# Performance work log

Measured on AMD Instinct MI355X. Metric: run time of the kernel, lower is better.

The kernel has to match this reference:

```python
import jax, jax.numpy as jnp
import numpy as np

BATCH = 16384
N_IN = 128
CTX = 128
H = 1024
NB = 8                      # num_bins
OUT_MULT = 3 * NB - 1       # widths + heights + derivatives for RQS
TAIL = 3.0                  # tail_bound
SCALE = float(np.sqrt((H * H) // 2))  # sqrt(prod(hidden_dims)//len(hidden_dims))
MIN_W = 1e-3; MIN_H = 1e-3; MIN_D = 1e-3
DPAD = float(np.log(np.exp(1.0 - MIN_D) - 1.0))  # softplus(DPAD)+MIN_D == 1 at boundaries


def _masks():
    # Standard sequential MADE masks. Input degrees 1..n_in, hidden degrees cycle.
    deg_in = np.arange(1, N_IN + 1)
    deg_h = (np.arange(H) % (N_IN - 1)) + 1
    m0 = deg_h[:, None] >= deg_in[None, :]          # [H, N_IN]
    m1 = deg_h[:, None] >= deg_h[None, :]           # [H, H]
    deg_out = np.repeat(deg_in, OUT_MULT)           # matches view(b, n_in, out_mult)
    m2 = deg_out[:, None] > deg_h[None, :]          # [N_IN*OUT_MULT, H]
    return jnp.asarray(m0), jnp.asarray(m1), jnp.asarray(m2)


def setup_inputs() -> dict:
    key = jax.random.key(0)
    k = jax.random.split(key, 6)
    def rn(kk, shape, fan_in):
        return (jax.random.normal(kk, shape, dtype=jnp.float32) * np.sqrt(1.0 / fan_in)).astype(jnp.float32)
    m0, m1, m2 = _masks()
    return {
        "x": jax.random.normal(k[0], (BATCH, N_IN), dtype=jnp.float32),
        "context": jax.random.normal(k[1], (BATCH, CTX), dtype=jnp.float32),
        "ctx_w": rn(k[2], (H, CTX), CTX),
        "w0": rn(k[3], (H, N_IN), N_IN), "b0": jnp.zeros((H,), jnp.float32),
        "w1": rn(k[4], (H, H), H),       "b1": jnp.zeros((H,), jnp.float32),
        "w2": rn(k[5], (N_IN * OUT_MULT, H), H), "b2": jnp.zeros((N_IN * OUT_MULT,), jnp.float32),
        "mask0": m0, "mask1": m1, "mask2": m2,
    }


def _rqs(x, uw, uh, ud):
    # x: [B, D]; uw, uh: [B, D, NB]; ud: [B, D, NB-1]
    inside = jnp.abs(x) <= TAIL
    xc = jnp.clip(x, -TAIL, TAIL)

    w = MIN_W + (1.0 - MIN_W * NB) * jax.nn.softmax(uw, axis=-1)
    cw = jnp.cumsum(w, axis=-1)
    cw = jnp.concatenate([jnp.zeros_like(cw[..., :1]), cw], axis=-1)
    cw = 2.0 * TAIL * cw - TAIL
    cw = cw.at[..., 0].set(-TAIL).at[..., -1].set(TAIL)
    widths = cw[..., 1:] - cw[..., :-1]

    h = MIN_H + (1.0 - MIN_H * NB) * jax.nn.softmax(uh, axis=-1)
    ch = jnp.cumsum(h, axis=-1)
    ch = jnp.concatenate([jnp.zeros_like(ch[..., :1]), ch], axis=-1)
    ch = 2.0 * TAIL * ch - TAIL
    ch = ch.at[..., 0].set(-TAIL).at[..., -1].set(TAIL)
    heights = ch[..., 1:] - ch[..., :-1]

    pad = jnp.full(ud.shape[:-1] + (1,), DPAD, ud.dtype)
    d = MIN_D + jax.nn.softplus(jnp.concatenate([pad, ud, pad], axis=-1))  # [B, D, NB+1]

    # bucketize: bin index per element (NB is small; comparison-sum beats searchsorted here)
    idx = jnp.clip(jnp.sum((xc[..., None] >= cw).astype(jnp.int32), axis=-1) - 1, 0, NB - 1)
    g = lambda a, i: jnp.take_along_axis(a, i[..., None], axis=-1)[..., 0]

    in_cw = g(cw, idx); in_w = g(widths, idx)
    in_ch = g(ch, idx); in_h = g(heights, idx)
    delta = in_h / in_w
    d0 = g(d, idx); d1 = g(d, idx + 1)

    theta = (xc - in_cw) / in_w
    t1m = theta * (1.0 - theta)
    denom = delta + (d0 + d1 - 2.0 * delta) * t1m
    num = in_h * (delta * theta * theta + d0 * t1m)
    y = in_ch + num / denom
    logdet = (2.0 * jnp.log(delta)
              + jnp.log(d1 * theta * theta + 2.0 * delta * t1m + d0 * (1.0 - theta) ** 2)
              - 2.0 * jnp.log(denom))

    y = jnp.where(inside, y, x)          # identity linear tails
    logdet = jnp.where(inside, logdet, 0.0)
    return y, logdet


def reference(x, context, ctx_w, w0, b0, w1, b1, w2, b2, mask0, mask1, mask2):
    m0 = mask0.astype(w0.dtype); m1 = mask1.astype(w1.dtype); m2 = mask2.astype(w2.dtype)
    hdn = jax.nn.relu(context @ ctx_w.T + x @ (w0 * m0).T + b0)
    hdn = jax.nn.relu(hdn @ (w1 * m1).T + b1)
    out = (hdn @ (w2 * m2).T + b2).reshape(-1, N_IN, OUT_MULT)
    uw = out[..., :NB] / SCALE
    uh = out[..., NB:2 * NB] / SCALE
    ud = out[..., 2 * NB:]
    y, ld = _rqs(x, uw, uh, ud)
    return y, jnp.sum(ld, axis=-1)
```

## Files before the change

kernel.cpp:

```cpp
#include <hip/hip_runtime.h>
#include <cstdint>
#include <cstddef>

#define BATCH   16384
#define N_IN    128
#define CTX     128
#define HDIM    1024
#define NB      8
#define OUT_MULT 23
#define OUT_PAD 24
#define NOUTP   (N_IN * OUT_PAD)
#define KCAT    (CTX + N_IN)

typedef __bf16 bf16x8 __attribute__((ext_vector_type(8)));
typedef float  f32x4  __attribute__((ext_vector_type(4)));

__device__ __forceinline__ uint16_t f2bf(float f) {
    union { float f; uint32_t u; } v; v.f = f;
    uint32_t u = v.u;
    u += 0x7FFFu + ((u >> 16) & 1u);
    return (uint16_t)(u >> 16);
}

__device__ __forceinline__ int kpref_dev(int d) {
    return (d <= 8) ? 9 * d : 72 + 8 * (d - 8);
}
__device__ __forceinline__ int dpos_dev(int p) {
    return (p < 72) ? (p / 9) : (8 + ((p - 72) >> 3));
}
__device__ __forceinline__ int h_of(int p) {
    if (p < 72) { int d = p / 9, j = p - 9 * d; return d + 127 * j; }
    int q = p - 72; int d = 8 + (q >> 3); int j = q & 7; return d + 127 * j;
}

__device__ __forceinline__ void async_ld16(const void* g, const void* l) {
    __builtin_amdgcn_global_load_lds(
        (__attribute__((address_space(1))) void*)(uintptr_t)g,
        (__attribute__((address_space(3))) void*)(uint32_t)(uintptr_t)l,
        16, 0, 0);
}


__global__ void pack_all(
    const float* __restrict__ x,    const float* __restrict__ ctx,
    const float* __restrict__ ctx_w,const float* __restrict__ w0,
    const float* __restrict__ b0,   const float* __restrict__ w1,
    const float* __restrict__ b1,   const float* __restrict__ w2,
    const float* __restrict__ b2,
    uint16_t* __restrict__ xcat, uint16_t* __restrict__ wcat,
    uint16_t* __restrict__ w1m,  uint16_t* __restrict__ w2p,
    float* __restrict__ b0p, float* __restrict__ b1p, float* __restrict__ b2p,
    float* __restrict__ ldz)
{
    __shared__ float srow[HDIM];
    const int blk = blockIdx.x;
    const int tid = threadIdx.x;

    if (blk < 4096) {
        int idx4 = (blk * 256 + tid) * 4;
        int b = idx4 >> 8, c = idx4 & 255;
        f32x4 v = (c < CTX) ? *(const f32x4*)(ctx + (b << 7) + c)
                            : *(const f32x4*)(x   + (b << 7) + (c - CTX));
        ushort4 o;
        o.x = f2bf(v[0]); o.y = f2bf(v[1]); o.z = f2bf(v[2]); o.w = f2bf(v[3]);
        *(ushort4*)(xcat + idx4) = o;
    } else if (blk < 5120) {
        int idx = (blk - 4096) * 256 + tid;
        int p = idx >> 8, c = idx & 255;
        int h = h_of(p);
        float v;
        if (c < CTX) v = ctx_w[(h << 7) + c];
        else {
            int col = c - CTX;
            v = (dpos_dev(p) >= col) ? w0[(h << 7) + col] : 0.0f;
        }
        wcat[idx] = f2bf(v);
    } else if (blk < 6144) {
        const int po = blk - 5120;
        const int drow = dpos_dev(po);
        const float* src = w1 + (size_t)h_of(po) * HDIM;
        *((f32x4*)srow + tid) = *((const f32x4*)src + tid);
        __syncthreads();
        ushort4 o;
#pragma unroll
        for (int e = 0; e < 4; ++e) {
            int pi = 4 * tid + e;
            float v = (drow >= dpos_dev(pi)) ? srow[h_of(pi)] : 0.0f;
            ((uint16_t*)&o)[e] = f2bf(v);
        }
        *((ushort4*)(w1m + (size_t)po * HDIM) + tid) = o;
    } else if (blk < 9216) {
        const int oo = blk - 6144;
        const int g = oo / OUT_PAD, t = oo - g * OUT_PAD;
        const bool live = (t < OUT_MULT);
        if (live) {
            const float* src = w2 + (size_t)(g * OUT_MULT + t) * HDIM;
            *((f32x4*)srow + tid) = *((const f32x4*)src + tid);
        }
        __syncthreads();
        ushort4 o;
#pragma unroll
        for (int e = 0; e < 4; ++e) {
            int pi = 4 * tid + e;
            float v = (live && g > dpos_dev(pi)) ? srow[h_of(pi)] : 0.0f;
            ((uint16_t*)&o)[e] = f2bf(v);
        }
        *((ushort4*)(w2p + (size_t)oo * HDIM) + tid) = o;
    } else if (blk < 9232) {
        int idx = (blk - 9216) * 256 + tid;
        if (idx < HDIM) {
            int h = h_of(idx);
            b0p[idx] = b0[h];
            b1p[idx] = b1[h];
        } else {
            int oo = idx - HDIM;
            int g = oo / OUT_PAD, t = oo - g * OUT_PAD;
            b2p[oo] = (t < OUT_MULT) ? b2[g * OUT_MULT + t] : 0.0f;
        }
    } else {
        int idx = (blk - 9232) * 256 + tid;
        ldz[idx] = 0.0f;
    }
}


template<int MODE>
__device__ __forceinline__ void gemm_bt_body(
    const uint16_t* __restrict__ A,
    const uint16_t* __restrict__ B,
    const float*    __restrict__ bias,
    uint16_t*       __restrict__ C,
    int N, int K, int NT)
{
    __shared__ __align__(16) uint16_t sA[2][128 * 64];
    __shared__ __align__(16) uint16_t sB[2][128 * 64];

    const int GM    = 64;
    const int per   = GM * NT;
    const int id    = blockIdx.x;
    const int grp   = id / per;
    const int rem   = id - grp * per;
    const int mt    = grp * GM + (rem & (GM - 1));
    const int nt    = (NT - 1) - (rem >> 6);
    const int bm    = mt << 7;
    const int bn    = nt << 7;

    int K_eff;
    if (MODE == 0)      { int dmax = dpos_dev(bn + 127); K_eff = 128 + dmax + 1; }
    else                { int dmax = dpos_dev(bn + 127); K_eff = kpref_dev(dmax + 1); }
    K_eff = min(K, (K_eff + 63) & ~63);

    const int tid   = threadIdx.x;
    const int wid   = tid >> 6;
    const int lane  = tid & 63;
    const int wm    = (wid & 1) << 6;
    const int wn    = (wid >> 1) << 6;
    const int lrow  = lane & 15;
    const int lquad = lane >> 4;

    const f32x4 vzero = {0.0f, 0.0f, 0.0f, 0.0f};
    f32x4 acc[4][4];
#pragma unroll
    for (int i = 0; i < 4; ++i)
#pragma unroll
        for (int j = 0; j < 4; ++j) acc[i][j] = vzero;

    int goff[4];
#pragma unroll
    for (int t = 0; t < 4; ++t) {
        int c = t * 256 + tid;
        int row = c >> 3, j = c & 7;
        int oct = j ^ (row & 7);
        goff[t] = row * K * 2 + oct * 16;
    }
    const char* gA = (const char*)(A + (size_t)bm * K);
    const char* gB = (const char*)(B + (size_t)bn * K);

    const int octx = lrow & 7;

    auto stage = [&](int b, int k0) {
        const int kb = k0 * 2;
#pragma unroll
        for (int t = 0; t < 4; ++t) {
            const int ldsoff = (t * 256 + (wid << 6)) * 16;
            async_ld16(gA + goff[t] + kb, (const char*)sA[b] + ldsoff);
            async_ld16(gB + goff[t] + kb, (const char*)sB[b] + ldsoff);
        }
    };

    stage(0, 0);
    __syncthreads();

    int cur = 0;
    for (int k0 = 0; k0 < K_eff; k0 += 64) {
        if (k0 + 64 < K_eff) stage(cur ^ 1, k0 + 64);

        const uint16_t* rA = sA[cur] + (wm + lrow) * 64;
        const uint16_t* rB = sB[cur] + (wn + lrow) * 64;
#pragma unroll
        for (int ks = 0; ks < 2; ++ks) {
            const int oct = ((ks << 2) | lquad) ^ octx;
            bf16x8 af[4], bfr[4];
#pragma unroll
            for (int i = 0; i < 4; ++i) af[i]  = *(const bf16x8*)(rA + i * 1024 + oct * 8);
#pragma unroll
            for (int j = 0; j < 4; ++j) bfr[j] = *(const bf16x8*)(rB + j * 1024 + oct * 8);
#pragma unroll
            for (int i = 0; i < 4; ++i)
#pragma unroll
                for (int j = 0; j < 4; ++j)
                    acc[i][j] = __builtin_amdgcn_mfma_f32_16x16x32_bf16(
                                    af[i], bfr[j], acc[i][j], 0, 0, 0);
        }

        __syncthreads();
        cur ^= 1;
    }

#pragma unroll
    for (int j = 0; j < 4; ++j) {
        const int col = bn + wn + j * 16 + lrow;
        const float bv = bias[col];
#pragma unroll
        for (int i = 0; i < 4; ++i) {
            const int row0 = bm + wm + i * 16 + (lquad << 2);
#pragma unroll
            for (int r = 0; r < 4; ++r) {
                float v = fmaxf(acc[i][j][r] + bv, 0.0f);
                C[(size_t)(row0 + r) * N + col] = f2bf(v);
            }
        }
    }
}

__global__ __launch_bounds__(256, 2) void gemm1_k(
    const uint16_t* __restrict__ A, const uint16_t* __restrict__ B,
    const float* __restrict__ bias, uint16_t* __restrict__ C,
    int N, int K, int NT)
{ gemm_bt_body<0>(A, B, bias, C, N, K, NT); }

__global__ __launch_bounds__(256, 2) void gemm2_k(
    const uint16_t* __restrict__ A, const uint16_t* __restrict__ B,
    const float* __restrict__ bias, uint16_t* __restrict__ C,
    int N, int K, int NT)
{ gemm_bt_body<1>(A, B, bias, C, N, K, NT); }


__device__ __forceinline__ float frcp(float v) { return __builtin_amdgcn_rcpf(v); }
__device__ __forceinline__ float softplusf(float v) {
    return fmaxf(v, 0.0f) + __logf(1.0f + __expf(-fabsf(v)));
}

__device__ __forceinline__ void spline_eval(const float* __restrict__ pp,
                                            float xv, float& yout, float& ldout)
{
    float p[OUT_PAD];
#pragma unroll
    for (int k = 0; k < OUT_PAD / 4; ++k)
        *(f32x4*)(p + 4 * k) = *(const f32x4*)(pp + 4 * k);

    const float TAILF = 3.0f;
    const float MIN_W = 0.001f, MIN_H = 0.001f, MIN_D = 0.001f;
    const float INV_SCALE = 1.0f / 724.0773439350246f;

    const float xc = fminf(fmaxf(xv, -TAILF), TAILF);

    float uw[NB], uh[NB];
#pragma unroll
    for (int k = 0; k < NB; ++k) { uw[k] = p[k] * INV_SCALE; uh[k] = p[NB + k] * INV_SCALE; }
    float mw = uw[0], mh = uh[0];
#pragma unroll
    for (int k = 1; k < NB; ++k) { mw = fmaxf(mw, uw[k]); mh = fmaxf(mh, uh[k]); }
    float ew[NB], eh[NB], sw = 0.0f, sh = 0.0f;
#pragma unroll
    for (int k = 0; k < NB; ++k) {
        ew[k] = __expf(uw[k] - mw); sw += ew[k];
        eh[k] = __expf(uh[k] - mh); sh += eh[k];
    }
    const float FACW = (1.0f - MIN_W * NB) * frcp(sw);
    const float FACH = (1.0f - MIN_H * NB) * frcp(sh);

    float cw[NB + 1], ch[NB + 1];
    cw[0] = -TAILF; ch[0] = -TAILF;
    float aw = 0.0f, ah = 0.0f;
#pragma unroll
    for (int k = 0; k < NB; ++k) {
        aw += MIN_W + FACW * ew[k];
        ah += MIN_H + FACH * eh[k];
        cw[k + 1] = (k == NB - 1) ? TAILF : 2.0f * TAILF * aw - TAILF;
        ch[k + 1] = (k == NB - 1) ? TAILF : 2.0f * TAILF * ah - TAILF;
    }

    float dd[NB + 1];
    dd[0]  = 1.0f;
    dd[NB] = 1.0f;
#pragma unroll
    for (int k = 1; k < NB; ++k) dd[k] = MIN_D + softplusf(p[2 * NB + (k - 1)]);

    float in_cw = cw[0], cw_n = cw[1], in_ch = ch[0], ch_n = ch[1];
    float d0 = dd[0], d1 = dd[1];
#pragma unroll
    for (int k = 1; k < NB; ++k) {
        const bool ge = (xc >= cw[k]);
        in_cw = ge ? cw[k]     : in_cw;
        cw_n  = ge ? cw[k + 1] : cw_n;
        in_ch = ge ? ch[k]     : in_ch;
        ch_n  = ge ? ch[k + 1] : ch_n;
        d0    = ge ? dd[k]     : d0;
        d1    = ge ? dd[k + 1] : d1;
    }
    const float in_w  = cw_n - in_cw;
    const float in_h  = ch_n - in_ch;
    const float inv_w = frcp(in_w);
    const float delta = in_h * inv_w;
    const float theta = (xc - in_cw) * inv_w;
    const float omt   = 1.0f - theta;
    const float t1m   = theta * omt;
    const float denom = delta + (d0 + d1 - 2.0f * delta) * t1m;
    const float num   = in_h * (delta * theta * theta + d0 * t1m);
    float yv = in_ch + num * frcp(denom);
    float ld = 2.0f * __logf(delta)
             + __logf(d1 * theta * theta + 2.0f * delta * t1m + d0 * omt * omt)
             - 2.0f * __logf(denom);
    const bool inside = fabsf(xv) <= TAILF;
    yout  = inside ? yv : xv;
    ldout = inside ? ld : 0.0f;
}


__global__ __launch_bounds__(256, 2) void gemm3_spline(
    const uint16_t* __restrict__ A,
    const uint16_t* __restrict__ B,
    const float*    __restrict__ bias,
    const float*    __restrict__ x,
    float* __restrict__ y,
    float* __restrict__ ldsum)
{
    __shared__ __align__(16) char smem[57344];
    float* ep = (float*)smem;

    const int NT  = 32;
    const int per = 64 * NT;
    const int id  = blockIdx.x;
    const int grp = id / per;
    const int rem = id - grp * per;
    const int mt  = grp * 64 + (rem & 63);
    const int nt  = 31 - (rem >> 6);
    const int bm  = mt << 7;
    const int bn  = nt * 96;

    const int K = HDIM;
    int K_eff = kpref_dev(4 * nt + 3);
    K_eff = min(K, (K_eff + 63) & ~63);

    const int tid   = threadIdx.x;
    const int wid   = tid >> 6;
    const int lane  = tid & 63;
    const int wm    = (wid & 1) << 6;
    const int wn    = (wid >> 1) * 48;
    const int lrow  = lane & 15;
    const int lquad = lane >> 4;

    const f32x4 vzero = {0.0f, 0.0f, 0.0f, 0.0f};
    f32x4 acc[4][3];
#pragma unroll
    for (int i = 0; i < 4; ++i)
#pragma unroll
        for (int j = 0; j < 3; ++j) acc[i][j] = vzero;

    int goffA[4], goffB[3];
#pragma unroll
    for (int t = 0; t < 4; ++t) {
        int c = t * 256 + tid;
        int row = c >> 3, j = c & 7;
        goffA[t] = row * K * 2 + (j ^ (row & 7)) * 16;
    }
#pragma unroll
    for (int t = 0; t < 3; ++t) {
        int c = t * 256 + tid;
        int row = c >> 3, j = c & 7;
        goffB[t] = row * K * 2 + (j ^ (row & 7)) * 16;
    }
    const char* gA = (const char*)(A + (size_t)bm * K);
    const char* gB = (const char*)(B + (size_t)bn * K);

    const int octx = lrow & 7;

    auto stage = [&](int b, int k0) {
        const int kb = k0 * 2;
        char* dA = smem + b * 16384;
        char* dB = smem + 32768 + b * 12288;
#pragma unroll
        for (int t = 0; t < 4; ++t) {
            const int ldsoff = (t * 256 + (wid << 6)) * 16;
            async_ld16(gA + goffA[t] + kb, dA + ldsoff);
            if (t < 3)
                async_ld16(gB + goffB[t] + kb, dB + ldsoff);
        }
    };

    stage(0, 0);
    __syncthreads();

    int cur = 0;
    for (int k0 = 0; k0 < K_eff; k0 += 64) {
        if (k0 + 64 < K_eff) stage(cur ^ 1, k0 + 64);

        const uint16_t* rA = (const uint16_t*)(smem + cur * 16384)
                             + (wm + lrow) * 64;
        const uint16_t* rB = (const uint16_t*)(smem + 32768 + cur * 12288)
                             + (wn + lrow) * 64;
#pragma unroll
        for (int ks = 0; ks < 2; ++ks) {
            const int oct = ((ks << 2) | lquad) ^ octx;
            bf16x8 af[4], bfr[3];
#pragma unroll
            for (int i = 0; i < 4; ++i) af[i]  = *(const bf16x8*)(rA + i * 1024 + oct * 8);
#pragma unroll
            for (int j = 0; j < 3; ++j) bfr[j] = *(const bf16x8*)(rB + j * 1024 + oct * 8);
#pragma unroll
            for (int i = 0; i < 4; ++i)
#pragma unroll
                for (int j = 0; j < 3; ++j)
                    acc[i][j] = __builtin_amdgcn_mfma_f32_16x16x32_bf16(
                                    af[i], bfr[j], acc[i][j], 0, 0, 0);
        }

        __syncthreads();
        cur ^= 1;
    }

#pragma unroll
    for (int ph = 0; ph < 2; ++ph) {
        if ((wid & 1) == ph) {
#pragma unroll
            for (int j = 0; j < 3; ++j) {
                const int col = wn + j * 16 + lrow;
                const float bv = bias[bn + col];
#pragma unroll
                for (int i = 0; i < 4; ++i) {
                    const int r0 = i * 16 + (lquad << 2);
#pragma unroll
                    for (int r = 0; r < 4; ++r)
                        ep[(r0 + r) * 100 + col] = acc[i][j][r] + bv;
                }
            }
        }
        __syncthreads();

        {
            const int row  = tid >> 2;
            const int sg   = tid & 3;
            const int grow = bm + (ph << 6) + row;
            const float xv = x[(size_t)grow * N_IN + (4 * nt + sg)];
            float yv, ld;
            spline_eval(ep + row * 100 + sg * OUT_PAD, xv, yv, ld);
            y[(size_t)grow * N_IN + 4 * nt + sg] = yv;

            ld += __shfl_xor(ld, 1, 64);
            ld += __shfl_xor(ld, 2, 64);
            if (sg == 0) atomicAdd(&ldsum[grow], ld);
        }
        if (ph == 0) __syncthreads();
    }
}


extern "C" void kernel_launch(void* const* d_in, const int* in_sizes, int n_in,
                              void* d_out, int out_size, void* d_ws, size_t ws_size,
                              hipStream_t stream)
{
    const float* x     = (const float*)d_in[0];
    const float* ctx   = (const float*)d_in[1];
    const float* ctx_w = (const float*)d_in[2];
    const float* w0    = (const float*)d_in[3];
    const float* b0    = (const float*)d_in[4];
    const float* w1    = (const float*)d_in[5];
    const float* b1    = (const float*)d_in[6];
    const float* w2    = (const float*)d_in[7];
    const float* b2    = (const float*)d_in[8];

    char* ws = (char*)d_ws;
    const size_t XCAT_B = (size_t)BATCH * KCAT * 2;
    const size_t H_B    = (size_t)BATCH * HDIM * 2;
    const size_t WCAT_B = (size_t)HDIM * KCAT * 2;
    const size_t W1_B   = (size_t)HDIM * HDIM * 2;
    const size_t W2P_B  = (size_t)NOUTP * HDIM * 2;

    uint16_t* xcat = (uint16_t*)(ws);
    uint16_t* h1   = (uint16_t*)(ws + XCAT_B);
    uint16_t* h2   = (uint16_t*)(ws + XCAT_B + H_B);
    uint16_t* wcat = (uint16_t*)(ws + XCAT_B + 2 * H_B);
    uint16_t* w1m  = (uint16_t*)(ws + XCAT_B + 2 * H_B + WCAT_B);
    uint16_t* w2p  = (uint16_t*)(ws + XCAT_B + 2 * H_B + WCAT_B + W1_B);
    float*    b0p  = (float*)   (ws + XCAT_B + 2 * H_B + WCAT_B + W1_B + W2P_B);
    float*    b1p  = b0p + HDIM;
    float*    b2p  = b1p + HDIM;

    float* yout  = (float*)d_out;
    float* ldout = yout + (size_t)BATCH * N_IN;

    pack_all<<<9296, 256, 0, stream>>>(x, ctx, ctx_w, w0, b0, w1, b1, w2, b2,
                                       xcat, wcat, w1m, w2p, b0p, b1p, b2p,
                                       ldout);

    const dim3 blk(256);
    gemm1_k<<<dim3(128 * (HDIM / 128)), blk, 0, stream>>>(
        xcat, wcat, b0p, h1, HDIM, KCAT, HDIM / 128);
    gemm2_k<<<dim3(128 * (HDIM / 128)), blk, 0, stream>>>(
        h1, w1m, b1p, h2, HDIM, HDIM, HDIM / 128);
    gemm3_spline<<<dim3(128 * 32), blk, 0, stream>>>(
        h2, w2p, b2p, x, yout, ldout);
}
```

Baseline: 229.6 us.

## Widen gemm3 N tile to 192 and drop LDS double buffering

The final GEMM+spline kernel's N tile grows from 96 to 192 columns, so each block handles 8 spline dimensions instead of 4 and the grid is halved. A-tile reuse doubles and per-warp accumulators double. The double-buffered async prefetch is replaced by a single-buffered load-sync-compute loop to fit the larger B tile in 40KB of LDS. The epilogue is split into four 32-row phases. The cost is that loads no longer overlap compute, and register pressure rises.

```diff
diff --git a/kernel.cpp b/kernel.cpp
--- a/kernel.cpp
+++ b/kernel.cpp
@@ -336,39 +336,41 @@
     float* __restrict__ y,
     float* __restrict__ ldsum)
 {
-    __shared__ __align__(16) char smem[57344];
-    float* ep = (float*)smem;
-
-    const int NT  = 32;
+    __shared__ __align__(16) char smem[40960];
+    uint16_t* sA = (uint16_t*)smem;
+    uint16_t* sB = (uint16_t*)(smem + 16384);
+    float* ep    = (float*)smem;
+
+    const int NT  = 16;
     const int per = 64 * NT;
     const int id  = blockIdx.x;
     const int grp = id / per;
     const int rem = id - grp * per;
     const int mt  = grp * 64 + (rem & 63);
-    const int nt  = 31 - (rem >> 6);
+    const int nt  = (NT - 1) - (rem >> 6);
     const int bm  = mt << 7;
-    const int bn  = nt * 96;
+    const int bn  = nt * 192;
 
     const int K = HDIM;
-    int K_eff = kpref_dev(4 * nt + 3);
+    int K_eff = kpref_dev(8 * nt + 7);
     K_eff = min(K, (K_eff + 63) & ~63);
 
     const int tid   = threadIdx.x;
     const int wid   = tid >> 6;
     const int lane  = tid & 63;
     const int wm    = (wid & 1) << 6;
-    const int wn    = (wid >> 1) * 48;
+    const int wn    = (wid >> 1) * 96;
     const int lrow  = lane & 15;
     const int lquad = lane >> 4;
 
     const f32x4 vzero = {0.0f, 0.0f, 0.0f, 0.0f};
-    f32x4 acc[4][3];
+    f32x4 acc[4][6];
 #pragma unroll
     for (int i = 0; i < 4; ++i)
 #pragma unroll
-        for (int j = 0; j < 3; ++j) acc[i][j] = vzero;
-
-    int goffA[4], goffB[3];
+        for (int j = 0; j < 6; ++j) acc[i][j] = vzero;
+
+    int goffA[4], goffB[6];
 #pragma unroll
     for (int t = 0; t < 4; ++t) {
         int c = t * 256 + tid;
@@ -376,7 +378,7 @@
         goffA[t] = row * K * 2 + (j ^ (row & 7)) * 16;
     }
 #pragma unroll
-    for (int t = 0; t < 3; ++t) {
+    for (int t = 0; t < 6; ++t) {
         int c = t * 256 + tid;
         int row = c >> 3, j = c & 7;
         goffB[t] = row * K * 2 + (j ^ (row & 7)) * 16;
@@ -385,83 +387,74 @@
     const char* gB = (const char*)(B + (size_t)bn * K);
 
     const int octx = lrow & 7;
-
-    auto stage = [&](int b, int k0) {
+    const uint16_t* rA = sA + (wm + lrow) * 64;
+    const uint16_t* rB = sB + (wn + lrow) * 64;
+
+    for (int k0 = 0; k0 < K_eff; k0 += 64) {
+        __syncthreads();
         const int kb = k0 * 2;
-        char* dA = smem + b * 16384;
-        char* dB = smem + 32768 + b * 12288;
-#pragma unroll
-        for (int t = 0; t < 4; ++t) {
+#pragma unroll
+        for (int t = 0; t < 6; ++t) {
             const int ldsoff = (t * 256 + (wid << 6)) * 16;
-            async_ld16(gA + goffA[t] + kb, dA + ldsoff);
-            if (t < 3)
-                async_ld16(gB + goffB[t] + kb, dB + ldsoff);
-        }
-    };
-
-    stage(0, 0);
-    __syncthreads();
-
-    int cur = 0;
-    for (int k0 = 0; k0 < K_eff; k0 += 64) {
-        if (k0 + 64 < K_eff) stage(cur ^ 1, k0 + 64);
-
-        const uint16_t* rA = (const uint16_t*)(smem + cur * 16384)
-                             + (wm + lrow) * 64;
-        const uint16_t* rB = (const uint16_t*)(smem + 32768 + cur * 12288)
-                             + (wn + lrow) * 64;
+            if (t < 4)
+                async_ld16(gA + goffA[t] + kb, (const char*)sA + ldsoff);
+            async_ld16(gB + goffB[t] + kb, (const char*)sB + ldsoff);
+        }
+        __syncthreads();
+
 #pragma unroll
         for (int ks = 0; ks < 2; ++ks) {
             const int oct = ((ks << 2) | lquad) ^ octx;
-            bf16x8 af[4], bfr[3];
+            bf16x8 af[4], bfr[6];
 #pragma unroll
             for (int i = 0; i < 4; ++i) af[i]  = *(const bf16x8*)(rA + i * 1024 + oct * 8);
 #pragma unroll
-            for (int j = 0; j < 3; ++j) bfr[j] = *(const bf16x8*)(rB + j * 1024 + oct * 8);
+            for (int j = 0; j < 6; ++j) bfr[j] = *(const bf16x8*)(rB + j * 1024 + oct * 8);
 #pragma unroll
             for (int i = 0; i < 4; ++i)
 #pragma unroll
-                for (int j = 0; j < 3; ++j)
+                for (int j = 0; j < 6; ++j)
                     acc[i][j] = __builtin_amdgcn_mfma_f32_16x16x32_bf16(
                                     af[i], bfr[j], acc[i][j], 0, 0, 0);
         }
-
-        __syncthreads();
-        cur ^= 1;
-    }
-
-#pragma unroll
-    for (int ph = 0; ph < 2; ++ph) {
-        if ((wid & 1) == ph) {
-#pragma unroll
-            for (int j = 0; j < 3; ++j) {
-                const int col = wn + j * 16 + lrow;
-                const float bv = bias[bn + col];
-#pragma unroll
-                for (int i = 0; i < 4; ++i) {
-                    const int r0 = i * 16 + (lquad << 2);
+    }
+
+    __syncthreads();
+
+#pragma unroll
+    for (int ph = 0; ph < 4; ++ph) {
+        if ((wid & 1) == (ph >> 1)) {
+#pragma unroll
+            for (int ii = 0; ii < 2; ++ii) {
+                const int i  = ((ph & 1) << 1) + ii;
+                const int l0 = (ii << 4) + (lquad << 2);
+#pragma unroll
+                for (int j = 0; j < 6; ++j) {
+                    const int col = wn + j * 16 + lrow;
+                    const float bv = bias[bn + col];
 #pragma unroll
                     for (int r = 0; r < 4; ++r)
-                        ep[(r0 + r) * 100 + col] = acc[i][j][r] + bv;
+                        ep[(l0 + r) * 196 + col] = acc[i][j][r] + bv;
                 }
             }
         }
         __syncthreads();
 
         {
-            const int row  = tid >> 2;
-            const int sg   = tid & 3;
-            const int grow = bm + (ph << 6) + row;
-            const float xv = x[(size_t)grow * N_IN + (4 * nt + sg)];
+            const int row  = tid >> 3;
+            const int sg   = tid & 7;
+            const int grow = bm + (ph << 5) + row;
+            const float xv = x[(size_t)grow * N_IN + (8 * nt + sg)];
             float yv, ld;
-            spline_eval(ep + row * 100 + sg * OUT_PAD, xv, yv, ld);
-            y[(size_t)grow * N_IN + 4 * nt + sg] = yv;
+            spline_eval(ep + row * 196 + sg * OUT_PAD, xv, yv, ld);
+            y[(size_t)grow * N_IN + 8 * nt + sg] = yv;
 
             ld += __shfl_xor(ld, 1, 64);
             ld += __shfl_xor(ld, 2, 64);
+            ld += __shfl_xor(ld, 4, 64);
             if (sg == 0) atomicAdd(&ldsum[grow], ld);
         }
-        if (ph == 0) __syncthreads();
+        if (ph < 3) __syncthreads();
     }
 }
 
@@ -509,6 +502,6 @@
         xcat, wcat, b0p, h1, HDIM, KCAT, HDIM / 128);
     gemm2_k<<<dim3(128 * (HDIM / 128)), blk, 0, stream>>>(
         h1, w1m, b1p, h2, HDIM, HDIM, HDIM / 128);
-    gemm3_spline<<<dim3(128 * 32), blk, 0, stream>>>(
+    gemm3_spline<<<dim3(128 * 16), blk, 0, stream>>>(
         h2, w2p, b2p, x, yout, ldout);
 }
```

Result: faster. 223.0 us (-2.9%).
